# Kernel tuning notes

Measured on AMD Instinct MI355X. Metric: run time of the kernel, lower is better.

Reference implementation:

```python
import jax, jax.numpy as jnp
from jax import lax
import numpy as np

INPUT_SIZE = 1000
HIDDEN = 128
SEQ = 22
NUM_CLASSES = 4
BATCH = 2048


def setup_inputs() -> dict:
    key = jax.random.key(0)
    ks = jax.random.split(key, 8)
    s_ih = 1.0 / np.sqrt(HIDDEN)
    inputs = jax.random.normal(ks[0], (BATCH, SEQ, INPUT_SIZE), dtype=jnp.float32)
    h0 = jax.random.normal(ks[1], (1, BATCH, HIDDEN), dtype=jnp.float32)  # init_hidden()
    W_ih = jax.random.uniform(ks[2], (3 * HIDDEN, INPUT_SIZE), jnp.float32, -s_ih, s_ih)
    W_hh = jax.random.uniform(ks[3], (3 * HIDDEN, HIDDEN), jnp.float32, -s_ih, s_ih)
    b_ih = jax.random.uniform(ks[4], (3 * HIDDEN,), jnp.float32, -s_ih, s_ih)
    b_hh = jax.random.uniform(ks[5], (3 * HIDDEN,), jnp.float32, -s_ih, s_ih)
    s_dec = 1.0 / np.sqrt(HIDDEN * SEQ)
    W_dec = jax.random.uniform(ks[6], (NUM_CLASSES, HIDDEN * SEQ), jnp.float32, -s_dec, s_dec)
    b_dec = jax.random.uniform(ks[7], (NUM_CLASSES,), jnp.float32, -s_dec, s_dec)
    return {"inputs": inputs, "h0": h0, "W_ih": W_ih, "W_hh": W_hh,
            "b_ih": b_ih, "b_hh": b_hh, "W_dec": W_dec, "b_dec": b_dec}


def reference(inputs, h0, W_ih, W_hh, b_ih, b_hh, W_dec, b_dec):
    B = inputs.shape[0]
    # Precompute input contribution for all timesteps: [B, T, 3H]
    x_gates = jnp.einsum('bti,gi->btg', inputs, W_ih) + b_ih

    def step(h, xg):  # h: [B,H], xg: [B,3H]
        hg = h @ W_hh.T + b_hh  # [B,3H]
        xr, xz, xn = jnp.split(xg, 3, axis=-1)
        hr, hz, hn = jnp.split(hg, 3, axis=-1)
        r = jax.nn.sigmoid(xr + hr)
        z = jax.nn.sigmoid(xz + hz)
        n = jnp.tanh(xn + r * hn)
        h_new = (1.0 - z) * n + z * h  # PyTorch GRU update
        return h_new, h_new

    _, outs = lax.scan(step, h0[0], jnp.swapaxes(x_gates, 0, 1))  # outs: [T,B,H]
    output = jnp.swapaxes(outs, 0, 1).reshape(B, SEQ * HIDDEN)  # [B, T*H]
    return output @ W_dec.T + b_dec  # [B, num_classes]
```

## Files before the change

### kernel.cpp

```cpp
#include <hip/hip_runtime.h>
#include <math.h>

#define BATCH 2048
#define SEQ   22
#define INSZ  1000
#define HID   128
#define G3    384
#define MTOT  (BATCH*SEQ)
#define KPAD  1024
#define DECW  (SEQ*HID)

typedef __attribute__((ext_vector_type(8))) short  bf16x8_t;
typedef __attribute__((ext_vector_type(4))) float  f32x4_t;
typedef __attribute__((ext_vector_type(8))) ushort us8_t;

typedef __attribute__((address_space(3))) ushort lds_us_t;
typedef __attribute__((address_space(1))) const ushort gbl_us_t;

__device__ inline void gload16(const ushort* g, ushort* l) {
    __builtin_amdgcn_global_load_lds((gbl_us_t*)g, (lds_us_t*)l, 16, 0, 0);
}

__device__ inline ushort bf16_rn(float x) {
    uint u = __float_as_uint(x);
    uint r = u + 0x7FFFu + ((u >> 16) & 1u);
    return (ushort)(r >> 16);
}
__device__ inline void split1(float a, ushort& h, ushort& l) {
    h = bf16_rn(a);
    const float fh = __uint_as_float(((uint)h) << 16);
    l = bf16_rn(a - fh);
}

__global__ __launch_bounds__(256)
void split_rows(const float* __restrict__ A, ushort* __restrict__ Hi,
                ushort* __restrict__ Lo, int nrows)
{
    const int nG = nrows * (KPAD / 8);
    for (int g = blockIdx.x * 256 + threadIdx.x; g < nG; g += gridDim.x * 256) {
        const int m = g >> 7;
        const int k = (g & 127) * 8;
        float4 v0 = make_float4(0.f, 0.f, 0.f, 0.f), v1 = v0;
        if (k < INSZ) {
            v0 = *(const float4*)&A[(size_t)m * INSZ + k];
            v1 = *(const float4*)&A[(size_t)m * INSZ + k + 4];
        }
        us8_t h, l;
        split1(v0.x, ((ushort*)&h)[0], ((ushort*)&l)[0]);
        split1(v0.y, ((ushort*)&h)[1], ((ushort*)&l)[1]);
        split1(v0.z, ((ushort*)&h)[2], ((ushort*)&l)[2]);
        split1(v0.w, ((ushort*)&h)[3], ((ushort*)&l)[3]);
        split1(v1.x, ((ushort*)&h)[4], ((ushort*)&l)[4]);
        split1(v1.y, ((ushort*)&h)[5], ((ushort*)&l)[5]);
        split1(v1.z, ((ushort*)&h)[6], ((ushort*)&l)[6]);
        split1(v1.w, ((ushort*)&h)[7], ((ushort*)&l)[7]);
        *(us8_t*)&Hi[(size_t)m * KPAD + k] = h;
        *(us8_t*)&Lo[(size_t)m * KPAD + k] = l;
    }
}

__global__ __launch_bounds__(256)
void mfma_gemm(const ushort* __restrict__ Ah, const ushort* __restrict__ Al,
               const ushort* __restrict__ Bh, const ushort* __restrict__ Bl,
               const float* __restrict__ bias, float* __restrict__ C)
{
    __shared__ ushort lds[4 * 128 * 32];

    const int tid  = threadIdx.x;
    const int lane = tid & 63;
    const int wid  = tid >> 6;

    const int d = blockIdx.x;
    const int xcd = d & 7, s = d >> 3;
    const int m0 = (xcd * 44 + s / 3) * 128;
    const int n0 = (s % 3) * 128;

    const int wm = (wid >> 1) * 64;
    const int wn = (wid & 1) * 64;

    const int seg0 = wid * 2;
    int rowS[2], chS[2];
#pragma unroll
    for (int i = 0; i < 2; ++i) {
        const int s_ = (seg0 + i) * 64 + lane;
        rowS[i] = s_ >> 2;
        chS[i]  = (s_ & 3) ^ ((rowS[i] >> 1) & 3);
    }

    f32x4_t acc[4][4];
#pragma unroll
    for (int i = 0; i < 4; ++i)
#pragma unroll
        for (int j = 0; j < 4; ++j) acc[i][j] = {0.f, 0.f, 0.f, 0.f};

    for (int kt = 0; kt < KPAD / 32; ++kt) {
        __syncthreads();
        const int kOff = kt * 32;
#pragma unroll
        for (int i = 0; i < 2; ++i) {
            const size_t goA = (size_t)(m0 + rowS[i]) * KPAD + kOff + chS[i] * 8;
            const size_t goB = (size_t)(n0 + rowS[i]) * KPAD + kOff + chS[i] * 8;
            const int lb = (seg0 + i) * 512;
            gload16(Ah + goA, &lds[lb]);
            gload16(Al + goA, &lds[4096 + lb]);
            gload16(Bh + goB, &lds[8192 + lb]);
            gload16(Bl + goB, &lds[12288 + lb]);
        }
        __syncthreads();

        bf16x8_t ah[4], al[4], bh[4], bl[4];
#pragma unroll
        for (int f = 0; f < 4; ++f) {
            {
                const int row = wm + f * 16 + (lane & 15);
                const int c   = (lane >> 4) ^ ((row >> 1) & 3);
                const int eo  = row * 32 + c * 8;
                ah[f] = *(const bf16x8_t*)&lds[eo];
                al[f] = *(const bf16x8_t*)&lds[4096 + eo];
            }
            {
                const int row = wn + f * 16 + (lane & 15);
                const int c   = (lane >> 4) ^ ((row >> 1) & 3);
                const int eo  = row * 32 + c * 8;
                bh[f] = *(const bf16x8_t*)&lds[8192 + eo];
                bl[f] = *(const bf16x8_t*)&lds[12288 + eo];
            }
        }
#pragma unroll
        for (int mf = 0; mf < 4; ++mf)
#pragma unroll
            for (int nf = 0; nf < 4; ++nf) {
                acc[mf][nf] = __builtin_amdgcn_mfma_f32_16x16x32_bf16(
                    ah[mf], bh[nf], acc[mf][nf], 0, 0, 0);
                acc[mf][nf] = __builtin_amdgcn_mfma_f32_16x16x32_bf16(
                    ah[mf], bl[nf], acc[mf][nf], 0, 0, 0);
                acc[mf][nf] = __builtin_amdgcn_mfma_f32_16x16x32_bf16(
                    al[mf], bh[nf], acc[mf][nf], 0, 0, 0);
            }
    }

#pragma unroll
    for (int nf = 0; nf < 4; ++nf) {
        const int gn = n0 + wn + nf * 16 + (lane & 15);
        const float bv = bias[gn];
#pragma unroll
        for (int mf = 0; mf < 4; ++mf) {
#pragma unroll
            for (int q = 0; q < 4; ++q) {
                const int gm = m0 + wm + mf * 16 + (lane >> 4) * 4 + q;
                C[(size_t)gm * G3 + gn] = acc[mf][nf][q] + bv;
            }
        }
    }
}

__global__ __launch_bounds__(256)
void transpose_whh(const float4* __restrict__ Whh4, float4* __restrict__ Wt4)
{
    const int idx = blockIdx.x * 256 + threadIdx.x;
    const int k4  = idx / G3;
    const int g   = idx - k4 * G3;
    Wt4[idx] = Whh4[g * 32 + k4];
}

__global__ __launch_bounds__(768)
void gru_scan_dec(const float* __restrict__ xg,
                  const float* __restrict__ h0,
                  const float4* __restrict__ Wt,
                  const float* __restrict__ b_hh,
                  const float* __restrict__ Wd,
                  const float* __restrict__ bd,
                  float* __restrict__ out)
{
    __shared__ float hs[8][132];
    __shared__ float pp[8][2][G3];
    __shared__ float outsL[8][DECW];

    const int tid = threadIdx.x;
    const int b0  = blockIdx.x << 3;
    const int jh  = tid / G3;
    const int g   = tid - jh * G3;

    float4 w[16];
#pragma unroll
    for (int q = 0; q < 16; ++q) w[q] = Wt[(jh * 16 + q) * G3 + g];
    const float addb = jh ? b_hh[g] : 0.f;

    for (int idx = tid; idx < 1024; idx += 768)
        hs[idx >> 7][idx & 127] = h0[((size_t)(b0 + (idx >> 7)) << 7) + (idx & 127)];
    __syncthreads();

    const int r_0 = tid >> 7,        j_0 = tid & 127;
    const int r_1 = (tid + 768) >> 7, j_1 = tid & 127;
    const bool has1 = (tid < 256);

    for (int t = 0; t < SEQ; ++t) {
        const size_t base0 = ((size_t)(b0 + r_0) * SEQ + t) * G3;
        const float xr0 = xg[base0 + j_0];
        const float xz0 = xg[base0 + 128 + j_0];
        const float xn0 = xg[base0 + 256 + j_0];
        float xr1 = 0.f, xz1 = 0.f, xn1 = 0.f;
        if (has1) {
            const size_t base1 = ((size_t)(b0 + r_1) * SEQ + t) * G3;
            xr1 = xg[base1 + j_1];
            xz1 = xg[base1 + 128 + j_1];
            xn1 = xg[base1 + 256 + j_1];
        }

        float acc[8] = {0.f, 0.f, 0.f, 0.f, 0.f, 0.f, 0.f, 0.f};
#pragma unroll
        for (int q = 0; q < 16; ++q) {
            const float4 wq = w[q];
            const int ho = (jh * 16 + q) << 2;
#pragma unroll
            for (int r = 0; r < 8; ++r) {
                const float4 h4 = *(const float4*)&hs[r][ho];
                acc[r] = fmaf(h4.x, wq.x, fmaf(h4.y, wq.y,
                         fmaf(h4.z, wq.z, fmaf(h4.w, wq.w, acc[r]))));
            }
        }
#pragma unroll
        for (int r = 0; r < 8; ++r) pp[r][jh][g] = acc[r] + addb;
        __syncthreads();

        {
            const float hr = pp[r_0][0][j_0]       + pp[r_0][1][j_0];
            const float hz = pp[r_0][0][128 + j_0] + pp[r_0][1][128 + j_0];
            const float hn = pp[r_0][0][256 + j_0] + pp[r_0][1][256 + j_0];
            const float rr = 1.f / (1.f + __expf(-(xr0 + hr)));
            const float zz = 1.f / (1.f + __expf(-(xz0 + hz)));
            float vv = xn0 + rr * hn;
            vv = fminf(fmaxf(vv, -20.f), 20.f);
            const float e2 = __expf(2.f * vv);
            const float nn = (e2 - 1.f) / (e2 + 1.f);
            const float hp = hs[r_0][j_0];
            const float hnew = fmaf(zz, hp - nn, nn);
            hs[r_0][j_0] = hnew;
            outsL[r_0][(t << 7) + j_0] = hnew;
        }
        if (has1) {
            const float hr = pp[r_1][0][j_1]       + pp[r_1][1][j_1];
            const float hz = pp[r_1][0][128 + j_1] + pp[r_1][1][128 + j_1];
            const float hn = pp[r_1][0][256 + j_1] + pp[r_1][1][256 + j_1];
            const float rr = 1.f / (1.f + __expf(-(xr1 + hr)));
            const float zz = 1.f / (1.f + __expf(-(xz1 + hz)));
            float vv = xn1 + rr * hn;
            vv = fminf(fmaxf(vv, -20.f), 20.f);
            const float e2 = __expf(2.f * vv);
            const float nn = (e2 - 1.f) / (e2 + 1.f);
            const float hp = hs[r_1][j_1];
            const float hnew = fmaf(zz, hp - nn, nn);
            hs[r_1][j_1] = hnew;
            outsL[r_1][(t << 7) + j_1] = hnew;
        }
        __syncthreads();
    }

    const int wv = tid >> 6, lane = tid & 63;
    if (wv < 8) {
        float da[4] = {0.f, 0.f, 0.f, 0.f};
        for (int i = 0; i < 44; ++i) {
            const float v = outsL[wv][i * 64 + lane];
#pragma unroll
            for (int c = 0; c < 4; ++c)
                da[c] = fmaf(v, Wd[(size_t)c * DECW + i * 64 + lane], da[c]);
        }
#pragma unroll
        for (int c = 0; c < 4; ++c) {
            float v = da[c];
            for (int off = 32; off > 0; off >>= 1) v += __shfl_down(v, off, 64);
            if (lane == 0) out[(b0 + wv) * 4 + c] = v + bd[c];
        }
    }
}

extern "C" void kernel_launch(void* const* d_in, const int* in_sizes, int n_in,
                              void* d_out, int out_size, void* d_ws, size_t ws_size,
                              hipStream_t stream)
{
    const float* inputs = (const float*)d_in[0];
    const float* h0     = (const float*)d_in[1];
    const float* W_ih   = (const float*)d_in[2];
    const float* W_hh   = (const float*)d_in[3];
    const float* b_ih   = (const float*)d_in[4];
    const float* b_hh   = (const float*)d_in[5];
    const float* W_dec  = (const float*)d_in[6];
    const float* b_dec  = (const float*)d_in[7];
    float* out = (float*)d_out;

    char* ws = (char*)d_ws;
    const size_t szAh = (size_t)MTOT * KPAD * 2;
    const size_t szB  = (size_t)G3 * KPAD * 2;
    ushort* A_hi = (ushort*)ws;
    ushort* A_lo = (ushort*)(ws + szAh);
    ushort* B_hi = (ushort*)(ws + 2 * szAh);
    ushort* B_lo = (ushort*)(ws + 2 * szAh + szB);
    float4* Wt   = (float4*)(ws + 2 * szAh + 2 * szB);
    float*  xgm  = (float*)(ws + 2 * szAh + 2 * szB + 196608);

    hipLaunchKernelGGL(split_rows, dim3(2048), dim3(256), 0, stream,
                       inputs, A_hi, A_lo, MTOT);
    hipLaunchKernelGGL(split_rows, dim3(192), dim3(256), 0, stream,
                       W_ih, B_hi, B_lo, G3);
    hipLaunchKernelGGL(transpose_whh, dim3(48), dim3(256), 0, stream,
                       (const float4*)W_hh, Wt);
    hipLaunchKernelGGL(mfma_gemm, dim3(1056), dim3(256), 0, stream,
                       A_hi, A_lo, B_hi, B_lo, b_ih, xgm);
    hipLaunchKernelGGL(gru_scan_dec, dim3(BATCH / 8), dim3(768), 0, stream,
                       xgm, h0, (const float4*)Wt, b_hh, W_dec, b_dec, out);
}
```

Before: 546.8 us.

## Fuse fp32-to-bf16 hi/lo split of inputs into double-buffered MFMA GEMM

Drops the separate split_rows pass over the large input tensor. The GEMM now loads fp32 inputs straight into LDS with an XOR swizzle and converts them to bf16 hi/lo pairs in registers just before the MFMAs. This removes a full read of the fp32 inputs plus a write and re-read of two bf16 copies. The GEMM loop also becomes double-buffered so the next K tile's loads overlap the current tile's MFMAs, at the cost of more LDS per block and extra conversion ALU work per tile. The last K tile clamps out-of-range column reads, which relies on the zero-padded B to cancel the duplicated values.

```diff
diff --git a/kernel.cpp b/kernel.cpp
--- a/kernel.cpp
+++ b/kernel.cpp
@@ -1,4 +1,5 @@
 #include <hip/hip_runtime.h>
+#include <hip/hip_bf16.h>
 #include <math.h>
 
 #define BATCH 2048
@@ -17,7 +18,10 @@
 typedef __attribute__((address_space(3))) ushort lds_us_t;
 typedef __attribute__((address_space(1))) const ushort gbl_us_t;
 
-__device__ inline void gload16(const ushort* g, ushort* l) {
+__device__ inline void gload16u(const ushort* g, ushort* l) {
+    __builtin_amdgcn_global_load_lds((gbl_us_t*)g, (lds_us_t*)l, 16, 0, 0);
+}
+__device__ inline void gload16f(const float* g, float* l) {
     __builtin_amdgcn_global_load_lds((gbl_us_t*)g, (lds_us_t*)l, 16, 0, 0);
 }
 
@@ -30,6 +34,26 @@
     h = bf16_rn(a);
     const float fh = __uint_as_float(((uint)h) << 16);
     l = bf16_rn(a - fh);
+}
+
+__device__ inline void cvt8(const float4 p0, const float4 p1,
+                            bf16x8_t& hi, bf16x8_t& lo)
+{
+    const float f[8] = {p0.x, p0.y, p0.z, p0.w, p1.x, p1.y, p1.z, p1.w};
+    union { uint u[4]; bf16x8_t v; } H, L;
+#pragma unroll
+    for (int i = 0; i < 4; ++i) {
+        const float2 v = make_float2(f[2 * i], f[2 * i + 1]);
+        __hip_bfloat162 h2 = __float22bfloat162_rn(v);
+        const uint w = *(const uint*)&h2;
+        H.u[i] = w;
+        const float fx = __uint_as_float(w << 16);
+        const float fy = __uint_as_float(w & 0xFFFF0000u);
+        const float2 r = make_float2(f[2 * i] - fx, f[2 * i + 1] - fy);
+        __hip_bfloat162 l2 = __float22bfloat162_rn(r);
+        L.u[i] = *(const uint*)&l2;
+    }
+    hi = H.v; lo = L.v;
 }
 
 __global__ __launch_bounds__(256)
@@ -59,12 +83,15 @@
     }
 }
 
-__global__ __launch_bounds__(256)
-void mfma_gemm(const ushort* __restrict__ Ah, const ushort* __restrict__ Al,
-               const ushort* __restrict__ Bh, const ushort* __restrict__ Bl,
+__global__ __launch_bounds__(256, 2)
+void mfma_gemm(const float* __restrict__ A,
+               const ushort* __restrict__ Bh,
+               const ushort* __restrict__ Bl,
                const float* __restrict__ bias, float* __restrict__ C)
 {
-    __shared__ ushort lds[4 * 128 * 32];
+    __shared__ float  ldsA[2][4096];
+    __shared__ ushort ldsBh[2][4096];
+    __shared__ ushort ldsBl[2][4096];
 
     const int tid  = threadIdx.x;
     const int lane = tid & 63;
@@ -78,14 +105,8 @@
     const int wm = (wid >> 1) * 64;
     const int wn = (wid & 1) * 64;
 
-    const int seg0 = wid * 2;
-    int rowS[2], chS[2];
-#pragma unroll
-    for (int i = 0; i < 2; ++i) {
-        const int s_ = (seg0 + i) * 64 + lane;
-        rowS[i] = s_ >> 2;
-        chS[i]  = (s_ & 3) ^ ((rowS[i] >> 1) & 3);
-    }
+    const int gcA = (lane & 7) ^ (lane >> 3);
+    const int chB = (lane & 3) ^ ((lane >> 3) & 3);
 
     f32x4_t acc[4][4];
 #pragma unroll
@@ -93,37 +114,50 @@
 #pragma unroll
         for (int j = 0; j < 4; ++j) acc[i][j] = {0.f, 0.f, 0.f, 0.f};
 
-    for (int kt = 0; kt < KPAD / 32; ++kt) {
-        __syncthreads();
-        const int kOff = kt * 32;
-#pragma unroll
-        for (int i = 0; i < 2; ++i) {
-            const size_t goA = (size_t)(m0 + rowS[i]) * KPAD + kOff + chS[i] * 8;
-            const size_t goB = (size_t)(n0 + rowS[i]) * KPAD + kOff + chS[i] * 8;
-            const int lb = (seg0 + i) * 512;
-            gload16(Ah + goA, &lds[lb]);
-            gload16(Al + goA, &lds[4096 + lb]);
-            gload16(Bh + goB, &lds[8192 + lb]);
-            gload16(Bl + goB, &lds[12288 + lb]);
-        }
-        __syncthreads();
+#define STAGE(KT, PB)                                                          \
+    {                                                                          \
+        const int kt_ = (KT);                                                  \
+        _Pragma("unroll")                                                      \
+        for (int u = 0; u < 4; ++u) {                                          \
+            const int rowA = wid * 32 + u * 8 + (lane >> 3);                   \
+            int gc = gcA;                                                      \
+            if (kt_ == 31 && gc >= 2) gc = 0;    \
+            gload16f(A + (size_t)(m0 + rowA) * INSZ + kt_ * 32 + gc * 4,       \
+                     &ldsA[PB][(wid * 4 + u) * 256 + lane * 4]);               \
+        }                                                                      \
+        _Pragma("unroll")                                                      \
+        for (int i = 0; i < 2; ++i) {                                          \
+            const int seg  = wid * 2 + i;                                      \
+            const int rowB = seg * 16 + (lane >> 2);                           \
+            const size_t go = (size_t)(n0 + rowB) * KPAD + kt_ * 32 + chB * 8; \
+            gload16u(Bh + go, &ldsBh[PB][seg * 512 + lane * 8]);               \
+            gload16u(Bl + go, &ldsBl[PB][seg * 512 + lane * 8]);               \
+        }                                                                      \
+    }
+
+    STAGE(0, 0);
+    __syncthreads();
+
+    for (int kt = 0; kt < 32; ++kt) {
+        const int cur = kt & 1;
+        if (kt < 31) STAGE(kt + 1, cur ^ 1);
 
         bf16x8_t ah[4], al[4], bh[4], bl[4];
 #pragma unroll
         for (int f = 0; f < 4; ++f) {
             {
                 const int row = wm + f * 16 + (lane & 15);
-                const int c   = (lane >> 4) ^ ((row >> 1) & 3);
-                const int eo  = row * 32 + c * 8;
-                ah[f] = *(const bf16x8_t*)&lds[eo];
-                al[f] = *(const bf16x8_t*)&lds[4096 + eo];
+                const int c2  = (lane >> 4) * 2;
+                const float4 p0 = *(const float4*)&ldsA[cur][row * 32 + ((c2)     ^ (row & 7)) * 4];
+                const float4 p1 = *(const float4*)&ldsA[cur][row * 32 + ((c2 + 1) ^ (row & 7)) * 4];
+                cvt8(p0, p1, ah[f], al[f]);
             }
             {
                 const int row = wn + f * 16 + (lane & 15);
                 const int c   = (lane >> 4) ^ ((row >> 1) & 3);
                 const int eo  = row * 32 + c * 8;
-                bh[f] = *(const bf16x8_t*)&lds[8192 + eo];
-                bl[f] = *(const bf16x8_t*)&lds[12288 + eo];
+                bh[f] = *(const bf16x8_t*)&ldsBh[cur][eo];
+                bl[f] = *(const bf16x8_t*)&ldsBl[cur][eo];
             }
         }
 #pragma unroll
@@ -137,7 +171,9 @@
                 acc[mf][nf] = __builtin_amdgcn_mfma_f32_16x16x32_bf16(
                     al[mf], bh[nf], acc[mf][nf], 0, 0, 0);
             }
-    }
+        __syncthreads();
+    }
+#undef STAGE
 
 #pragma unroll
     for (int nf = 0; nf < 4; ++nf) {
@@ -190,7 +226,7 @@
         hs[idx >> 7][idx & 127] = h0[((size_t)(b0 + (idx >> 7)) << 7) + (idx & 127)];
     __syncthreads();
 
-    const int r_0 = tid >> 7,        j_0 = tid & 127;
+    const int r_0 = tid >> 7,         j_0 = tid & 127;
     const int r_1 = (tid + 768) >> 7, j_1 = tid & 127;
     const bool has1 = (tid < 256);
 
@@ -289,23 +325,18 @@
     float* out = (float*)d_out;
 
     char* ws = (char*)d_ws;
-    const size_t szAh = (size_t)MTOT * KPAD * 2;
-    const size_t szB  = (size_t)G3 * KPAD * 2;
-    ushort* A_hi = (ushort*)ws;
-    ushort* A_lo = (ushort*)(ws + szAh);
-    ushort* B_hi = (ushort*)(ws + 2 * szAh);
-    ushort* B_lo = (ushort*)(ws + 2 * szAh + szB);
-    float4* Wt   = (float4*)(ws + 2 * szAh + 2 * szB);
-    float*  xgm  = (float*)(ws + 2 * szAh + 2 * szB + 196608);
-
-    hipLaunchKernelGGL(split_rows, dim3(2048), dim3(256), 0, stream,
-                       inputs, A_hi, A_lo, MTOT);
+    const size_t szB = (size_t)G3 * KPAD * 2;
+    ushort* B_hi = (ushort*)ws;
+    ushort* B_lo = (ushort*)(ws + szB);
+    float4* Wt   = (float4*)(ws + 2 * szB);
+    float*  xgm  = (float*)(ws + 2 * szB + 196608);
+
     hipLaunchKernelGGL(split_rows, dim3(192), dim3(256), 0, stream,
                        W_ih, B_hi, B_lo, G3);
     hipLaunchKernelGGL(transpose_whh, dim3(48), dim3(256), 0, stream,
                        (const float4*)W_hh, Wt);
     hipLaunchKernelGGL(mfma_gemm, dim3(1056), dim3(256), 0, stream,
-                       A_hi, A_lo, B_hi, B_lo, b_ih, xgm);
+                       inputs, B_hi, B_lo, b_ih, xgm);
     hipLaunchKernelGGL(gru_scan_dec, dim3(BATCH / 8), dim3(768), 0, stream,
                        xgm, h0, (const float4*)Wt, b_hh, W_dec, b_dec, out);
 }
```

Measured after the change: 509.0 us. 1.07x faster.
